# Kernel tuning notes

Measured on AMD Instinct MI355X. Metric: run time of the kernel, lower is better.

Reference implementation:

```python
import jax, jax.numpy as jnp
import numpy as np

B, N, FIN = 4, 4096, 128
H, U = 4, 32

def setup_inputs() -> dict:
    key = jax.random.key(0)
    k = jax.random.split(key, 6)
    x = jax.random.normal(k[0], (B, N, FIN), dtype=jnp.float32)
    adj = (jax.random.uniform(k[1], (B, N, N)) < 0.05).astype(jnp.float32)
    glorot = lambda kk, shape, fi, fo: jax.random.uniform(kk, shape, jnp.float32,
                                                          -np.sqrt(6.0/(fi+fo)), np.sqrt(6.0/(fi+fo)))
    W = glorot(k[2], (FIN, H*U), FIN, H*U)
    a_src = glorot(k[3], (H, U, 1), U, 1)
    a_dst = glorot(k[4], (H, U, 1), U, 1)
    bias = jnp.zeros((H*U,), dtype=jnp.float32)
    return {"x": x, "adj": adj, "W": W, "a_src": a_src, "a_dst": a_dst, "bias": bias}

def reference(x, adj, W, a_src, a_dst, bias):
    # inference mode: attention dropout is a no-op
    b, n, _ = x.shape
    h_heads, u = a_src.shape[0], a_src.shape[1]
    # add self-loops, clip to {0,1}
    adj = jnp.clip(adj + jnp.eye(n, dtype=adj.dtype)[None], 0.0, 1.0)
    h = (x @ W).reshape(b, n, h_heads, u).transpose(0, 2, 1, 3)      # [B,H,N,U]
    f1 = jnp.einsum('bhnu,hu->bhn', h, a_src[..., 0])                # [B,H,N]
    f2 = jnp.einsum('bhnu,hu->bhn', h, a_dst[..., 0])                # [B,H,N]
    e = f1[:, :, :, None] + f2[:, :, None, :]                        # [B,H,N,N]
    e = jnp.where(e > 0, e, 0.2 * e)                                 # LeakyReLU(0.2)
    e = jnp.where(adj[:, None] > 0.0, e, jnp.float32(-1e9))
    alpha = jax.nn.softmax(e, axis=-1)
    out = jnp.einsum('bhij,bhju->bhiu', alpha, h)                    # [B,H,N,U]
    out = out.transpose(0, 2, 1, 3).reshape(b, n, h_heads * u) + bias
    return jnp.where(out > 0, out, jnp.expm1(out))                   # ELU
```

## Files before the change

### kernel.cpp

```cpp
#include <hip/hip_runtime.h>
#include <math.h>

#define NB   4
#define NN   4096
#define FIN  128
#define FOUT 128
#define NH   4
#define UU   32

#define K1_ROWS 64
#define K1_RT   8
#define K1_CT   4
#define XPAD    132

__global__ __launch_bounds__(256) void k1_feat(
    const float* __restrict__ x, const float* __restrict__ W,
    const float* __restrict__ a_src, const float* __restrict__ a_dst,
    float* __restrict__ hfeat, float* __restrict__ f1g, float* __restrict__ f2g)
{
    __shared__ __align__(16) float Wq[32 * FOUT];
    __shared__ __align__(16) float xs[K1_ROWS * XPAD];

    const int tid  = threadIdx.x;
    const int row0 = blockIdx.x * K1_ROWS;

    const float4* x4 = (const float4*)(x + (size_t)row0 * FIN);
    for (int idx = tid; idx < K1_ROWS * FIN / 4; idx += 256) {
        int r = idx >> 5, q = idx & 31;
        *(float4*)(xs + r * XPAD + q * 4) = x4[idx];
    }

    const int cg = tid & 31;
    const int rg = tid >> 5;
    float acc[K1_RT][K1_CT];
    #pragma unroll
    for (int rr = 0; rr < K1_RT; rr++)
        #pragma unroll
        for (int cc = 0; cc < K1_CT; cc++) acc[rr][cc] = 0.f;

    for (int kt = 0; kt < 4; kt++) {
        __syncthreads();
        for (int idx = tid; idx < 32 * FOUT / 4; idx += 256)
            ((float4*)Wq)[idx] = ((const float4*)W)[kt * 1024 + idx];
        __syncthreads();
        #pragma unroll
        for (int k4 = 0; k4 < 8; k4++) {
            const int kb = kt * 32 + k4 * 4;
            float4 xv[K1_RT];
            #pragma unroll
            for (int rr = 0; rr < K1_RT; rr++)
                xv[rr] = *(const float4*)(xs + (rg * K1_RT + rr) * XPAD + kb);
            #pragma unroll
            for (int kk = 0; kk < 4; kk++) {
                float wv[K1_CT];
                #pragma unroll
                for (int cc = 0; cc < K1_CT; cc++)
                    wv[cc] = Wq[(k4 * 4 + kk) * FOUT + cg + 32 * cc];
                #pragma unroll
                for (int rr = 0; rr < K1_RT; rr++) {
                    float xk = ((const float*)&xv[rr])[kk];
                    #pragma unroll
                    for (int cc = 0; cc < K1_CT; cc++)
                        acc[rr][cc] = fmaf(xk, wv[cc], acc[rr][cc]);
                }
            }
        }
    }
    __syncthreads();
    #pragma unroll
    for (int rr = 0; rr < K1_RT; rr++)
        #pragma unroll
        for (int cc = 0; cc < K1_CT; cc++)
            xs[(rg * K1_RT + rr) * XPAD + cg + 32 * cc] = acc[rr][cc];
    __syncthreads();

    float4* h4 = (float4*)(hfeat + (size_t)row0 * FOUT);
    for (int idx = tid; idx < K1_ROWS * FOUT / 4; idx += 256) {
        int r = idx >> 5, q = idx & 31;
        h4[idx] = *(const float4*)(xs + r * XPAD + q * 4);
    }

    for (int task = tid; task < K1_ROWS * NH * 2; task += 256) {
        int row = task >> 3;
        int head = (task >> 1) & 3;
        int which = task & 1;
        const float* av = which ? a_dst : a_src;
        float s = 0.f;
        #pragma unroll
        for (int u = 0; u < UU; u++)
            s += xs[row * XPAD + head * UU + u] * av[head * UU + u];
        float* dst = which ? f2g : f1g;
        dst[(size_t)(row0 + row) * NH + head] = s;
    }
}

#define CAP  512
#define APAD 516
#define PPAD 132

__global__ __launch_bounds__(256) void k2_gat(
    const float* __restrict__ adj, const float* __restrict__ hfeat,
    const float* __restrict__ f1g, const float* __restrict__ f2g,
    const float* __restrict__ bias, float* __restrict__ out)
{
    const int row  = blockIdx.x;
    const int b    = row >> 12;
    const int i    = row & (NN - 1);
    const int tid  = threadIdx.x;
    const int lane = tid & 63;
    const int wv   = tid >> 6;

    __shared__ int   nbr[CAP];
    __shared__ float alpha[NH][APAD];
    __shared__ float part[8][PPAD];
    __shared__ float inv_s[NH];
    __shared__ int   cnt_s;

    if (tid == 0) cnt_s = 0;
    __syncthreads();

    const float4* arow = (const float4*)(adj + (size_t)row * NN);
    float4 v[4];
    #pragma unroll
    for (int it = 0; it < 4; it++)
        v[it] = arow[wv * 256 + it * 64 + lane];

    const unsigned long long below = (1ull << lane) - 1ull;
    #pragma unroll
    for (int it = 0; it < 4; it++) {
        const int jb = (wv * 256 + it * 64 + lane) << 2;
        const bool p0 = (v[it].x > 0.f) | (jb + 0 == i);
        const bool p1 = (v[it].y > 0.f) | (jb + 1 == i);
        const bool p2 = (v[it].z > 0.f) | (jb + 2 == i);
        const bool p3 = (v[it].w > 0.f) | (jb + 3 == i);
        unsigned long long m0 = __ballot(p0), m1 = __ballot(p1);
        unsigned long long m2 = __ballot(p2), m3 = __ballot(p3);
        int c0 = __popcll(m0), c1 = __popcll(m1), c2 = __popcll(m2), c3 = __popcll(m3);
        int base = 0;
        if (lane == 0) base = atomicAdd(&cnt_s, c0 + c1 + c2 + c3);
        base = __shfl(base, 0, 64);
        if (p0) { int p = base + __popcll(m0 & below);                if (p < CAP) nbr[p] = jb + 0; }
        if (p1) { int p = base + c0 + __popcll(m1 & below);           if (p < CAP) nbr[p] = jb + 1; }
        if (p2) { int p = base + c0 + c1 + __popcll(m2 & below);      if (p < CAP) nbr[p] = jb + 2; }
        if (p3) { int p = base + c0 + c1 + c2 + __popcll(m3 & below); if (p < CAP) nbr[p] = jb + 3; }
    }
    __syncthreads();
    const int K = (cnt_s < CAP) ? cnt_s : CAP;

    const float4 f1v = ((const float4*)f1g)[row];
    for (int k = tid; k < K; k += 256) {
        int j = nbr[k];
        float4 f2v = ((const float4*)f2g)[(size_t)b * NN + j];
        float e0 = f1v.x + f2v.x; e0 = e0 > 0.f ? e0 : 0.2f * e0;
        float e1 = f1v.y + f2v.y; e1 = e1 > 0.f ? e1 : 0.2f * e1;
        float e2 = f1v.z + f2v.z; e2 = e2 > 0.f ? e2 : 0.2f * e2;
        float e3 = f1v.w + f2v.w; e3 = e3 > 0.f ? e3 : 0.2f * e3;
        alpha[0][k] = e0; alpha[1][k] = e1; alpha[2][k] = e2; alpha[3][k] = e3;
    }
    __syncthreads();

    {
        float m = -1e30f;
        for (int k = lane; k < K; k += 64) m = fmaxf(m, alpha[wv][k]);
        #pragma unroll
        for (int off = 32; off > 0; off >>= 1) m = fmaxf(m, __shfl_xor(m, off, 64));
        float s = 0.f;
        for (int k = lane; k < K; k += 64) {
            float a = __expf(alpha[wv][k] - m);
            alpha[wv][k] = a;
            s += a;
        }
        #pragma unroll
        for (int off = 32; off > 0; off >>= 1) s += __shfl_xor(s, off, 64);
        if (lane == 0) inv_s[wv] = 1.f / s;
    }
    __syncthreads();

    const int cq = tid & 31;
    const int kg = tid >> 5;
    const int hh = cq >> 3;
    const float* hb = hfeat + (size_t)b * NN * FOUT + cq * 4;
    float4 acc = make_float4(0.f, 0.f, 0.f, 0.f);
    int k = kg;
    for (; k + 8 < K; k += 16) {
        int j0 = nbr[k], j1 = nbr[k + 8];
        float a0 = alpha[hh][k], a1 = alpha[hh][k + 8];
        float4 h0 = *(const float4*)(hb + (size_t)j0 * FOUT);
        float4 h1 = *(const float4*)(hb + (size_t)j1 * FOUT);
        acc.x = fmaf(a0, h0.x, acc.x); acc.y = fmaf(a0, h0.y, acc.y);
        acc.z = fmaf(a0, h0.z, acc.z); acc.w = fmaf(a0, h0.w, acc.w);
        acc.x = fmaf(a1, h1.x, acc.x); acc.y = fmaf(a1, h1.y, acc.y);
        acc.z = fmaf(a1, h1.z, acc.z); acc.w = fmaf(a1, h1.w, acc.w);
    }
    if (k < K) {
        int j0 = nbr[k];
        float a0 = alpha[hh][k];
        float4 h0 = *(const float4*)(hb + (size_t)j0 * FOUT);
        acc.x = fmaf(a0, h0.x, acc.x); acc.y = fmaf(a0, h0.y, acc.y);
        acc.z = fmaf(a0, h0.z, acc.z); acc.w = fmaf(a0, h0.w, acc.w);
    }
    *(float4*)&part[kg][cq * 4] = acc;
    __syncthreads();

    if (tid < FOUT) {
        float o = 0.f;
        #pragma unroll
        for (int g = 0; g < 8; g++) o += part[g][tid];
        o = o * inv_s[tid >> 5] + bias[tid];
        o = o > 0.f ? o : expm1f(o);
        out[(size_t)row * FOUT + tid] = o;
    }
}

extern "C" void kernel_launch(void* const* d_in, const int* in_sizes, int n_in,
                              void* d_out, int out_size, void* d_ws, size_t ws_size,
                              hipStream_t stream) {
    const float* x     = (const float*)d_in[0];
    const float* adj   = (const float*)d_in[1];
    const float* W     = (const float*)d_in[2];
    const float* a_src = (const float*)d_in[3];
    const float* a_dst = (const float*)d_in[4];
    const float* bias  = (const float*)d_in[5];
    float* out = (float*)d_out;

    char* ws = (char*)d_ws;
    float* hfeat = (float*)ws;
    float* f1g   = (float*)(ws + (size_t)NB * NN * FOUT * 4);
    float* f2g   = f1g + (size_t)NB * NN * NH;

    k1_feat<<<NB * NN / K1_ROWS, 256, 0, stream>>>(x, W, a_src, a_dst, hfeat, f1g, f2g);
    k2_gat<<<NB * NN, 256, 0, stream>>>(adj, hfeat, f1g, f2g, bias, out);
}
```

Baseline: 420.3 us.

## Replace sparse neighbor-gather GAT with dense flash-style MFMA attention using split bf16

```diff
diff --git a/kernel.cpp b/kernel.cpp
--- a/kernel.cpp
+++ b/kernel.cpp
@@ -8,6 +8,18 @@
 #define NH   4
 #define UU   32
 
+typedef short bf16x8 __attribute__((ext_vector_type(8)));
+typedef float f32x4  __attribute__((ext_vector_type(4)));
+
+__device__ __forceinline__ unsigned short f2bf(float v) {
+    unsigned int u = __float_as_uint(v);
+    unsigned int r = u + 0x7fffu + ((u >> 16) & 1u);
+    return (unsigned short)(r >> 16);
+}
+__device__ __forceinline__ float bf2f(unsigned short s) {
+    return __uint_as_float(((unsigned int)s) << 16);
+}
+
 #define K1_ROWS 64
 #define K1_RT   8
 #define K1_CT   4
@@ -16,7 +28,8 @@
 __global__ __launch_bounds__(256) void k1_feat(
     const float* __restrict__ x, const float* __restrict__ W,
     const float* __restrict__ a_src, const float* __restrict__ a_dst,
-    float* __restrict__ hfeat, float* __restrict__ f1g, float* __restrict__ f2g)
+    unsigned short* __restrict__ hhi, unsigned short* __restrict__ hlo,
+    float* __restrict__ f1g, float* __restrict__ f2T)
 {
     __shared__ __align__(16) float Wq[32 * FOUT];
     __shared__ __align__(16) float xs[K1_ROWS * XPAD];
@@ -74,10 +87,18 @@
             xs[(rg * K1_RT + rr) * XPAD + cg + 32 * cc] = acc[rr][cc];
     __syncthreads();
 
-    float4* h4 = (float4*)(hfeat + (size_t)row0 * FOUT);
-    for (int idx = tid; idx < K1_ROWS * FOUT / 4; idx += 256) {
-        int r = idx >> 5, q = idx & 31;
-        h4[idx] = *(const float4*)(xs + r * XPAD + q * 4);
+    const int bb = row0 >> 12;
+    const int ib = row0 & (NN - 1);
+
+    for (int idx = tid; idx < FOUT * K1_ROWS; idx += 256) {
+        int col = idx >> 6;
+        int r   = idx & 63;
+        float v = xs[r * XPAD + col];
+        unsigned short hb = f2bf(v);
+        unsigned short lb = f2bf(v - bf2f(hb));
+        size_t o = ((size_t)bb * FOUT + col) * NN + (size_t)(ib + r);
+        hhi[o] = hb;
+        hlo[o] = lb;
     }
 
     for (int task = tid; task < K1_ROWS * NH * 2; task += 256) {
@@ -89,126 +110,143 @@
         #pragma unroll
         for (int u = 0; u < UU; u++)
             s += xs[row * XPAD + head * UU + u] * av[head * UU + u];
-        float* dst = which ? f2g : f1g;
-        dst[(size_t)(row0 + row) * NH + head] = s;
-    }
-}
-
-#define CAP  512
-#define APAD 516
-#define PPAD 132
-
-__global__ __launch_bounds__(256) void k2_gat(
-    const float* __restrict__ adj, const float* __restrict__ hfeat,
-    const float* __restrict__ f1g, const float* __restrict__ f2g,
-    const float* __restrict__ bias, float* __restrict__ out)
+        if (which) f2T[((size_t)bb * NH + head) * NN + (size_t)(ib + row)] = s;
+        else       f1g[(size_t)(row0 + row) * NH + head] = s;
+    }
+}
+
+__global__ __launch_bounds__(512, 4) void k2_flash(
+    const float* __restrict__ adj,
+    const unsigned short* __restrict__ hhi,
+    const unsigned short* __restrict__ hlo,
+    const float* __restrict__ f1g,
+    const float* __restrict__ f2T,
+    const float* __restrict__ bias,
+    float* __restrict__ out)
 {
-    const int row  = blockIdx.x;
-    const int b    = row >> 12;
-    const int i    = row & (NN - 1);
+    const int blk  = blockIdx.x;
+    const int xcd  = blk & 7;
+    const int b    = xcd >> 1;
+    const int itile = (blk >> 3) | ((xcd & 1) << 6);
+    const int i0   = itile << 5;
     const int tid  = threadIdx.x;
     const int lane = tid & 63;
-    const int wv   = tid >> 6;
-
-    __shared__ int   nbr[CAP];
-    __shared__ float alpha[NH][APAD];
-    __shared__ float part[8][PPAD];
-    __shared__ float inv_s[NH];
-    __shared__ int   cnt_s;
-
-    if (tid == 0) cnt_s = 0;
-    __syncthreads();
-
-    const float4* arow = (const float4*)(adj + (size_t)row * NN);
-    float4 v[4];
+    const int w    = tid >> 6;
+    const int h    = w & 3;
+    const int isub = (w & 4) << 2;
+    const int r16  = lane & 15;
+    const int ksl  = lane >> 4;
+
+    const int irow = i0 + isub + r16;
+    const size_t grow = (size_t)b * NN + irow;
+
+    const float* adjp = adj + grow * NN + ksl * 8;
+    const float* f2p  = f2T + ((size_t)b * NH + h) * NN + ksl * 8;
+    const float  f1i  = f1g[grow * NH + h];
+    const int    uc   = h * UU + r16;
+    const unsigned short* ph0 = hhi + ((size_t)b * FOUT + uc) * NN + ksl * 8;
+    const unsigned short* ph1 = ph0 + (size_t)16 * NN;
+    const unsigned short* pl0 = hlo + ((size_t)b * FOUT + uc) * NN + ksl * 8;
+    const unsigned short* pl1 = pl0 + (size_t)16 * NN;
+
+    f32x4 c0 = {0.f, 0.f, 0.f, 0.f};
+    f32x4 c1 = {0.f, 0.f, 0.f, 0.f};
+    float m_run = 0.f;
+    float l_run = 0.f;
+    const int sbase = ksl << 2;
+
+    for (int jb = 0; jb < NN; jb += 32) {
+        float4 a0  = *(const float4*)(adjp + jb);
+        float4 a1  = *(const float4*)(adjp + jb + 4);
+        float4 f20 = *(const float4*)(f2p + jb);
+        float4 f21 = *(const float4*)(f2p + jb + 4);
+        bf16x8 bh0 = *(const bf16x8*)(ph0 + jb);
+        bf16x8 bh1 = *(const bf16x8*)(ph1 + jb);
+        bf16x8 bl0 = *(const bf16x8*)(pl0 + jb);
+        bf16x8 bl1 = *(const bf16x8*)(pl1 + jb);
+
+        const int jdiff = irow - jb - ksl * 8;
+        float s[8];
+        {
+            const float* av = (const float*)&a0;
+            const float* fv = (const float*)&f20;
+            #pragma unroll
+            for (int e = 0; e < 4; e++) {
+                float t = f1i + fv[e];
+                t = fmaxf(t, 0.2f * t);
+                s[e] = ((av[e] > 0.f) | (e == jdiff)) ? t : -1e9f;
+            }
+            const float* av2 = (const float*)&a1;
+            const float* fv2 = (const float*)&f21;
+            #pragma unroll
+            for (int e = 0; e < 4; e++) {
+                float t = f1i + fv2[e];
+                t = fmaxf(t, 0.2f * t);
+                s[e + 4] = ((av2[e] > 0.f) | ((e + 4) == jdiff)) ? t : -1e9f;
+            }
+        }
+
+        float mt = fmaxf(fmaxf(fmaxf(s[0], s[1]), fmaxf(s[2], s[3])),
+                         fmaxf(fmaxf(s[4], s[5]), fmaxf(s[6], s[7])));
+        mt = fmaxf(mt, __shfl_xor(mt, 16, 64));
+        mt = fmaxf(mt, __shfl_xor(mt, 32, 64));
+
+        if (!__all(mt <= m_run + 8.f)) {
+            float m_new = fmaxf(m_run, mt);
+            float sc = __expf(m_run - m_new);
+            m_run = m_new;
+            l_run *= sc;
+            #pragma unroll
+            for (int rg = 0; rg < 4; rg++) {
+                float scr = __shfl(sc, sbase + rg, 64);
+                c0[rg] *= scr;
+                c1[rg] *= scr;
+            }
+        }
+
+        float p[8];
+        float lsum = 0.f;
+        #pragma unroll
+        for (int e = 0; e < 8; e++) {
+            p[e] = __expf(s[e] - m_run);
+            lsum += p[e];
+        }
+        l_run += lsum;
+
+        bf16x8 pa, pb;
+        #pragma unroll
+        for (int e = 0; e < 8; e++) {
+            unsigned short hb = f2bf(p[e]);
+            pa[e] = (short)hb;
+            pb[e] = (short)f2bf(p[e] - bf2f(hb));
+        }
+
+        c0 = __builtin_amdgcn_mfma_f32_16x16x32_bf16(pa, bh0, c0, 0, 0, 0);
+        c1 = __builtin_amdgcn_mfma_f32_16x16x32_bf16(pa, bh1, c1, 0, 0, 0);
+        c0 = __builtin_amdgcn_mfma_f32_16x16x32_bf16(pb, bh0, c0, 0, 0, 0);
+        c1 = __builtin_amdgcn_mfma_f32_16x16x32_bf16(pb, bh1, c1, 0, 0, 0);
+        c0 = __builtin_amdgcn_mfma_f32_16x16x32_bf16(pa, bl0, c0, 0, 0, 0);
+        c1 = __builtin_amdgcn_mfma_f32_16x16x32_bf16(pa, bl1, c1, 0, 0, 0);
+    }
+
+    float l = l_run;
+    l += __shfl_xor(l, 16, 64);
+    l += __shfl_xor(l, 32, 64);
+    const float inv = 1.f / l;
+
+    const float bias0 = bias[h * UU + r16];
+    const float bias1 = bias[h * UU + 16 + r16];
     #pragma unroll
-    for (int it = 0; it < 4; it++)
-        v[it] = arow[wv * 256 + it * 64 + lane];
-
-    const unsigned long long below = (1ull << lane) - 1ull;
-    #pragma unroll
-    for (int it = 0; it < 4; it++) {
-        const int jb = (wv * 256 + it * 64 + lane) << 2;
-        const bool p0 = (v[it].x > 0.f) | (jb + 0 == i);
-        const bool p1 = (v[it].y > 0.f) | (jb + 1 == i);
-        const bool p2 = (v[it].z > 0.f) | (jb + 2 == i);
-        const bool p3 = (v[it].w > 0.f) | (jb + 3 == i);
-        unsigned long long m0 = __ballot(p0), m1 = __ballot(p1);
-        unsigned long long m2 = __ballot(p2), m3 = __ballot(p3);
-        int c0 = __popcll(m0), c1 = __popcll(m1), c2 = __popcll(m2), c3 = __popcll(m3);
-        int base = 0;
-        if (lane == 0) base = atomicAdd(&cnt_s, c0 + c1 + c2 + c3);
-        base = __shfl(base, 0, 64);
-        if (p0) { int p = base + __popcll(m0 & below);                if (p < CAP) nbr[p] = jb + 0; }
-        if (p1) { int p = base + c0 + __popcll(m1 & below);           if (p < CAP) nbr[p] = jb + 1; }
-        if (p2) { int p = base + c0 + c1 + __popcll(m2 & below);      if (p < CAP) nbr[p] = jb + 2; }
-        if (p3) { int p = base + c0 + c1 + c2 + __popcll(m3 & below); if (p < CAP) nbr[p] = jb + 3; }
-    }
-    __syncthreads();
-    const int K = (cnt_s < CAP) ? cnt_s : CAP;
-
-    const float4 f1v = ((const float4*)f1g)[row];
-    for (int k = tid; k < K; k += 256) {
-        int j = nbr[k];
-        float4 f2v = ((const float4*)f2g)[(size_t)b * NN + j];
-        float e0 = f1v.x + f2v.x; e0 = e0 > 0.f ? e0 : 0.2f * e0;
-        float e1 = f1v.y + f2v.y; e1 = e1 > 0.f ? e1 : 0.2f * e1;
-        float e2 = f1v.z + f2v.z; e2 = e2 > 0.f ? e2 : 0.2f * e2;
-        float e3 = f1v.w + f2v.w; e3 = e3 > 0.f ? e3 : 0.2f * e3;
-        alpha[0][k] = e0; alpha[1][k] = e1; alpha[2][k] = e2; alpha[3][k] = e3;
-    }
-    __syncthreads();
-
-    {
-        float m = -1e30f;
-        for (int k = lane; k < K; k += 64) m = fmaxf(m, alpha[wv][k]);
-        #pragma unroll
-        for (int off = 32; off > 0; off >>= 1) m = fmaxf(m, __shfl_xor(m, off, 64));
-        float s = 0.f;
-        for (int k = lane; k < K; k += 64) {
-            float a = __expf(alpha[wv][k] - m);
-            alpha[wv][k] = a;
-            s += a;
-        }
-        #pragma unroll
-        for (int off = 32; off > 0; off >>= 1) s += __shfl_xor(s, off, 64);
-        if (lane == 0) inv_s[wv] = 1.f / s;
-    }
-    __syncthreads();
-
-    const int cq = tid & 31;
-    const int kg = tid >> 5;
-    const int hh = cq >> 3;
-    const float* hb = hfeat + (size_t)b * NN * FOUT + cq * 4;
-    float4 acc = make_float4(0.f, 0.f, 0.f, 0.f);
-    int k = kg;
-    for (; k + 8 < K; k += 16) {
-        int j0 = nbr[k], j1 = nbr[k + 8];
-        float a0 = alpha[hh][k], a1 = alpha[hh][k + 8];
-        float4 h0 = *(const float4*)(hb + (size_t)j0 * FOUT);
-        float4 h1 = *(const float4*)(hb + (size_t)j1 * FOUT);
-        acc.x = fmaf(a0, h0.x, acc.x); acc.y = fmaf(a0, h0.y, acc.y);
-        acc.z = fmaf(a0, h0.z, acc.z); acc.w = fmaf(a0, h0.w, acc.w);
-        acc.x = fmaf(a1, h1.x, acc.x); acc.y = fmaf(a1, h1.y, acc.y);
-        acc.z = fmaf(a1, h1.z, acc.z); acc.w = fmaf(a1, h1.w, acc.w);
-    }
-    if (k < K) {
-        int j0 = nbr[k];
-        float a0 = alpha[hh][k];
-        float4 h0 = *(const float4*)(hb + (size_t)j0 * FOUT);
-        acc.x = fmaf(a0, h0.x, acc.x); acc.y = fmaf(a0, h0.y, acc.y);
-        acc.z = fmaf(a0, h0.z, acc.z); acc.w = fmaf(a0, h0.w, acc.w);
-    }
-    *(float4*)&part[kg][cq * 4] = acc;
-    __syncthreads();
-
-    if (tid < FOUT) {
-        float o = 0.f;
-        #pragma unroll
-        for (int g = 0; g < 8; g++) o += part[g][tid];
-        o = o * inv_s[tid >> 5] + bias[tid];
-        o = o > 0.f ? o : expm1f(o);
-        out[(size_t)row * FOUT + tid] = o;
+    for (int rg = 0; rg < 4; rg++) {
+        float invr = __shfl(inv, sbase + rg, 64);
+        int r = isub + sbase + rg;
+        size_t orow = ((size_t)b * NN + (size_t)(i0 + r)) * FOUT;
+        float o0 = c0[rg] * invr + bias0;
+        o0 = o0 > 0.f ? o0 : expm1f(o0);
+        out[orow + h * UU + r16] = o0;
+        float o1 = c1[rg] * invr + bias1;
+        o1 = o1 > 0.f ? o1 : expm1f(o1);
+        out[orow + h * UU + 16 + r16] = o1;
     }
 }
 
@@ -223,11 +261,11 @@
     const float* bias  = (const float*)d_in[5];
     float* out = (float*)d_out;
 
-    char* ws = (char*)d_ws;
-    float* hfeat = (float*)ws;
-    float* f1g   = (float*)(ws + (size_t)NB * NN * FOUT * 4);
-    float* f2g   = f1g + (size_t)NB * NN * NH;
-
-    k1_feat<<<NB * NN / K1_ROWS, 256, 0, stream>>>(x, W, a_src, a_dst, hfeat, f1g, f2g);
-    k2_gat<<<NB * NN, 256, 0, stream>>>(adj, hfeat, f1g, f2g, bias, out);
-}
+    unsigned short* hhi = (unsigned short*)d_ws;
+    unsigned short* hlo = hhi + (size_t)NB * FOUT * NN;
+    float* f1g = (float*)(hlo + (size_t)NB * FOUT * NN);
+    float* f2T = f1g + (size_t)NB * NN * NH;
+
+    k1_feat<<<NB * NN / K1_ROWS, 256, 0, stream>>>(x, W, a_src, a_dst, hhi, hlo, f1g, f2T);
+    k2_flash<<<512, 512, 0, stream>>>(adj, hhi, hlo, f1g, f2T, bias, out);
+}
```

Result: slower. 706.7 us (+68.1%).
